# Kernel optimization log

Measured on AMD Instinct MI355X. Metric: run time of the kernel, lower is better.

Reference implementation:

```python
import jax, jax.numpy as jnp
import numpy as np

# Module hyperparameters (from init_kwargs)
C = 128        # in_channel
L = 16         # seq_len
K = 7          # filter_size
DIL = 1        # dilation
G = 4          # num_groups
SPAN = (K - 1) * DIL + 1
PAD = (SPAN - 1) // 2

B, H, W = 8, 56, 56


def setup_inputs() -> dict:
    key = jax.random.key(0)
    k1, k2 = jax.random.split(key)
    x = jax.random.normal(k1, (B, C, L, H, W), dtype=jnp.float32)
    # kaiming_normal(mode='fan_out', nonlinearity='relu'):
    # fan_out = shape[0] * K * K, std = sqrt(2 / fan_out)
    std = (2.0 / (C * K * K)) ** 0.5
    filter_weight = jax.random.normal(k2, (C, L, K, K), dtype=jnp.float32) * std
    return {"x": x, "filter_weight": filter_weight}


def reference(x, filter_weight):
    # x: (B, C, T, H, W) ; filter_weight: (C, T, K, K)
    b, c, t, h, w = x.shape
    # zero-pad spatial dims
    x2 = jnp.pad(x, ((0, 0), (0, 0), (0, 0), (PAD, PAD), (PAD, PAD)))
    # x1: temporally shifted input (frame t-1, first frame duplicated)
    x1 = jnp.concatenate([x[:, :, :1], x[:, :, :-1]], axis=2)

    outs = []
    # static K*K offset loop (dy slow, dx fast -> matches torch meshgrid 'ij' flatten order)
    for dy in range(0, SPAN, DIL):
        for dx in range(0, SPAN, DIL):
            w_ct = filter_weight[:, :, dy // DIL, dx // DIL]  # (C, T)
            shifted = jax.lax.slice(
                x2, (0, 0, 0, dy, dx), (b, c, t, dy + h, dx + w))
            prod = w_ct[None, :, :, None, None] * x1 * shifted  # (B,C,T,H,W)
            # groupwise channel mean -> (B, G, T, H, W)
            resp = prod.reshape(b, G, c // G, t, h, w).mean(axis=2)
            outs.append(resp)
    # concat over offsets along channel dim -> (B, K^2*G, T, H, W)
    return jnp.concatenate(outs, axis=1)
```

## Files before the change

kernel.cpp:

```cpp
#include <hip/hip_runtime.h>
#include <cstdint>

#define C_ 128
#define L_ 16
#define G_ 4
#define H_ 56
#define W_ 56
#define HW_ 3136
#define CH_ 4
#define NCK_ 8
#define RS_ 64
#define NROW_ 10
#define XS_F (CH_ * NROW_ * RS_)
#define XTASK_ (CH_ * NROW_ * 16)
#define WL_F 2048
#define NBUF_ 2
#define LDS_F (WL_F + NBUF_ * XS_F)

typedef float f4 __attribute__((ext_vector_type(4)));
typedef __attribute__((address_space(3))) uint32_t lds_u32;
typedef const __attribute__((address_space(1))) uint32_t glb_u32;

__global__ __launch_bounds__(256, 2)
void wcorr(const float* __restrict__ x, const float* __restrict__ wgt,
           float* __restrict__ out) {
  __shared__ float lds[LDS_F];

  int bid = blockIdx.x;
  int wid = (bid & 7) * 896 + (bid >> 3);
  int htile = wid % 14;
  int rest = wid / 14;
  int t = rest & 15;
  int bg = rest >> 4;
  int g = bg & 3;
  int b = bg >> 2;
  int h0 = htile * 4;

  int tid = threadIdx.x;
  int tx = tid & 7;
  int slot = tid >> 3;
  int h = slot & 3;
  int dy = slot >> 2;
  bool active = (dy < 7) && (tx < 7);
  int dyc = dy < 7 ? dy : 6;
  int txc = tx < 7 ? tx : 6;
  int r = h + dyc;
  int t1 = t > 0 ? t - 1 : 0;
  int w0 = 8 * txc;

  for (int i = WL_F + tid; i < LDS_F; i += 256) lds[i] = 0.0f;
  __syncthreads();

  const size_t cstride = (size_t)L_ * HW_;
  const float* xg = x + ((size_t)b * C_ + (size_t)g * 32) * cstride;
  const float* x1b = xg + (size_t)t1 * HW_ + (size_t)(h0 + h) * W_ + w0;

  {
    const float sc = 1.0f / 32.0f;
    const float* wsrc = wgt + (size_t)(g * 32) * (L_ * 49) + t * 49;
    #pragma unroll
    for (int j = 0; j < 8; ++j) {
      int idx = tid + j * 256;
      int c = idx >> 6;
      int rem = idx & 63;
      int dyy = rem >> 3, dxx = rem & 7;
      float v = 0.0f;
      if (dyy < 7 && dxx < 7)
        v = wsrc[(size_t)c * (L_ * 49) + dyy * 7 + dxx] * sc;
      lds[idx] = v;
    }
  }

  auto stage = [&](int tau, int fb, int c0, bool on) {
    int row = tau >> 4;
    int sb = tau & 15;
    int ci = (row * 205) >> 11;
    int rr = row - ci * 10;
    int vb = sb ^ (rr & 7);
    int hh = h0 - 3 + rr;
    bool ok = on && (vb >= 1) && (vb <= 14) && (hh >= 0) && (hh < H_);
    const float* src = xg + (size_t)(c0 + ci) * cstride + (size_t)t * HW_
                          + hh * W_ + (vb * 4 - 4);
    float* dst = &lds[fb + (tau & ~63) * 4];
    if (ok)
      __builtin_amdgcn_global_load_lds((glb_u32*)src, (lds_u32*)dst, 16, 0, 0);
  };
  auto stage_chunk = [&](int fb, int c0) {
    stage(tid, fb, c0, true);
    stage(tid + 256, fb, c0, true);
    stage(tid + 512, fb, c0, tid + 512 < XTASK_);
  };

  float acc[7][8];
  #pragma unroll
  for (int i = 0; i < 7; ++i)
    #pragma unroll
    for (int p = 0; p < 8; ++p) acc[i][p] = 0.0f;

  stage_chunk(WL_F, 0);

  #pragma unroll 1
  for (int k = 0; k < NCK_; ++k) {
    __syncthreads();
    if (k + 1 < NCK_)
      stage_chunk(WL_F + ((k + 1) & 1) * XS_F, (k + 1) * CH_);

    int fb = WL_F + (k & 1) * XS_F;
    int c0 = k * CH_;
    int s = r & 7;
    #pragma unroll
    for (int ci = 0; ci < CH_; ++ci) {
      const f4* xsrow = (const f4*)&lds[fb + (ci * NROW_ + r) * RS_];
      f4 q0 = xsrow[(2 * txc + 0) ^ s];
      f4 q1 = xsrow[(2 * txc + 1) ^ s];
      f4 q2 = xsrow[(2 * txc + 2) ^ s];
      f4 q3 = xsrow[(2 * txc + 3) ^ s];
      const f4* wl = (const f4*)&lds[(c0 + ci) * 64 + dyc * 8];
      f4 wv0 = wl[0];
      f4 wv1 = wl[1];
      const float* x1p = x1b + (size_t)(c0 + ci) * cstride;
      f4 a0 = *(const f4*)(x1p);
      f4 a1 = *(const f4*)(x1p + 4);
      float w7[7] = {wv0.x, wv0.y, wv0.z, wv0.w, wv1.x, wv1.y, wv1.z};
      float rr_[16] = {q0.x, q0.y, q0.z, q0.w, q1.x, q1.y, q1.z, q1.w,
                       q2.x, q2.y, q2.z, q2.w, q3.x, q3.y, q3.z, q3.w};
      float x1v[8] = {a0.x, a0.y, a0.z, a0.w, a1.x, a1.y, a1.z, a1.w};
      #pragma unroll
      for (int dxx = 0; dxx < 7; ++dxx) {
        #pragma unroll
        for (int p = 0; p < 8; ++p) {
          acc[dxx][p] = fmaf(w7[dxx], x1v[p] * rr_[p + dxx + 1], acc[dxx][p]);
        }
      }
    }
  }

  if (active) {
    #pragma unroll
    for (int dxx = 0; dxx < 7; ++dxx) {
      int och = (dy * 7 + dxx) * G_ + g;
      float* op = out + (((size_t)b * 196 + och) * L_ + t) * (size_t)HW_
                      + (size_t)(h0 + h) * W_ + w0;
      f4 o0 = {acc[dxx][0], acc[dxx][1], acc[dxx][2], acc[dxx][3]};
      f4 o1 = {acc[dxx][4], acc[dxx][5], acc[dxx][6], acc[dxx][7]};
      __builtin_nontemporal_store(o0, (f4*)op);
      __builtin_nontemporal_store(o1, (f4*)(op + 4));
    }
  }
}

extern "C" void kernel_launch(void* const* d_in, const int* in_sizes, int n_in,
                              void* d_out, int out_size, void* d_ws, size_t ws_size,
                              hipStream_t stream) {
  const float* x = (const float*)d_in[0];
  const float* w = (const float*)d_in[1];
  float* o = (float*)d_out;
  dim3 grid(7168), block(256);
  hipLaunchKernelGGL(wcorr, grid, block, 0, stream, x, w, o);
}
```

Baseline: 232.9 us.

## Give each wavefront a private LDS staging buffer and replace block barriers with vmcnt waits

Each wavefront now stages only the input rows it needs (5 rows per channel) into its own double-buffered LDS region. This removes the per-chunk __syncthreads, with each wave using s_waitcnt vmcnt to wait only on its own async global-to-LDS loads. The chunk size drops from 4 to 2 channels, and the x1 global loads are issued before staging so they overlap. Adjacent waves overlap in rows, so some input is loaded redundantly. Correctness also depends on the hand-counted vmcnt values matching the number of outstanding loads.

```diff
diff --git a/kernel.cpp b/kernel.cpp
--- a/kernel.cpp
+++ b/kernel.cpp
@@ -7,15 +7,13 @@
 #define H_ 56
 #define W_ 56
 #define HW_ 3136
-#define CH_ 4
-#define NCK_ 8
-#define RS_ 64
-#define NROW_ 10
-#define XS_F (CH_ * NROW_ * RS_)
-#define XTASK_ (CH_ * NROW_ * 16)
+#define CH_ 2
+#define NCK_ 16
+#define NR_ 5
+#define WBUF_F (CH_ * NR_ * 64)
 #define WL_F 2048
-#define NBUF_ 2
-#define LDS_F (WL_F + NBUF_ * XS_F)
+#define LDS_F (WL_F + 4 * 2 * WBUF_F)
+#define XT_ (CH_ * NR_ * 16)
 
 typedef float f4 __attribute__((ext_vector_type(4)));
 typedef __attribute__((address_space(3))) uint32_t lds_u32;
@@ -37,6 +35,8 @@
   int h0 = htile * 4;
 
   int tid = threadIdx.x;
+  int lane = tid & 63;
+  int wvu = __builtin_amdgcn_readfirstlane(tid >> 6);
   int tx = tid & 7;
   int slot = tid >> 3;
   int h = slot & 3;
@@ -45,15 +45,11 @@
   int dyc = dy < 7 ? dy : 6;
   int txc = tx < 7 ? tx : 6;
   int r = h + dyc;
+  int lr = r - 2 * wvu;
   int t1 = t > 0 ? t - 1 : 0;
   int w0 = 8 * txc;
 
   for (int i = WL_F + tid; i < LDS_F; i += 256) lds[i] = 0.0f;
-  __syncthreads();
-
-  const size_t cstride = (size_t)L_ * HW_;
-  const float* xg = x + ((size_t)b * C_ + (size_t)g * 32) * cstride;
-  const float* x1b = xg + (size_t)t1 * HW_ + (size_t)(h0 + h) * W_ + w0;
 
   {
     const float sc = 1.0f / 32.0f;
@@ -71,24 +67,26 @@
     }
   }
 
-  auto stage = [&](int tau, int fb, int c0, bool on) {
+  const size_t cstride = (size_t)L_ * HW_;
+  const float* xg = x + ((size_t)b * C_ + (size_t)g * 32) * cstride;
+  const float* x1b = xg + (size_t)t1 * HW_ + (size_t)(h0 + h) * W_ + w0;
+
+  auto stage = [&](int call, int kb, int c0) {
+    int tau = lane + call * 64;
     int row = tau >> 4;
     int sb = tau & 15;
-    int ci = (row * 205) >> 11;
-    int rr = row - ci * 10;
-    int vb = sb ^ (rr & 7);
-    int hh = h0 - 3 + rr;
-    bool ok = on && (vb >= 1) && (vb <= 14) && (hh >= 0) && (hh < H_);
+    int ci = (row >= NR_) ? 1 : 0;
+    int lrr = row - ci * NR_;
+    int rg = 2 * wvu + lrr;
+    int vb = sb ^ (rg & 7);
+    int hh = h0 - 3 + rg;
+    bool ok = (tau < XT_) && (vb >= 1) && (vb <= 14) && (rg <= 9)
+              && (hh >= 0) && (hh < H_);
     const float* src = xg + (size_t)(c0 + ci) * cstride + (size_t)t * HW_
                           + hh * W_ + (vb * 4 - 4);
-    float* dst = &lds[fb + (tau & ~63) * 4];
+    float* dst = &lds[WL_F + (wvu * 2 + kb) * WBUF_F + call * 256];
     if (ok)
       __builtin_amdgcn_global_load_lds((glb_u32*)src, (lds_u32*)dst, 16, 0, 0);
-  };
-  auto stage_chunk = [&](int fb, int c0) {
-    stage(tid, fb, c0, true);
-    stage(tid + 256, fb, c0, true);
-    stage(tid + 512, fb, c0, tid + 512 < XTASK_);
   };
 
   float acc[7][8];
@@ -97,20 +95,36 @@
     #pragma unroll
     for (int p = 0; p < 8; ++p) acc[i][p] = 0.0f;
 
-  stage_chunk(WL_F, 0);
+  __syncthreads();
 
+  stage(0, 0, 0); stage(1, 0, 0); stage(2, 0, 0);
+
+  int s = r & 7;
   #pragma unroll 1
   for (int k = 0; k < NCK_; ++k) {
-    __syncthreads();
-    if (k + 1 < NCK_)
-      stage_chunk(WL_F + ((k + 1) & 1) * XS_F, (k + 1) * CH_);
+    __builtin_amdgcn_sched_barrier(0);
+    int c0 = k * CH_;
+    int kb = k & 1;
+    const float* x1p0 = x1b + (size_t)(c0 + 0) * cstride;
+    const float* x1p1 = x1b + (size_t)(c0 + 1) * cstride;
+    f4 a00 = *(const f4*)(x1p0);
+    f4 a01 = *(const f4*)(x1p0 + 4);
+    f4 a10 = *(const f4*)(x1p1);
+    f4 a11 = *(const f4*)(x1p1 + 4);
+    if (k + 1 < NCK_) {
+      stage(0, kb ^ 1, c0 + CH_);
+      stage(1, kb ^ 1, c0 + CH_);
+      stage(2, kb ^ 1, c0 + CH_);
+      asm volatile("s_waitcnt vmcnt(6)");
+    } else {
+      asm volatile("s_waitcnt vmcnt(4)");
+    }
+    __builtin_amdgcn_sched_barrier(0);
 
-    int fb = WL_F + (k & 1) * XS_F;
-    int c0 = k * CH_;
-    int s = r & 7;
+    const float* base = &lds[WL_F + (wvu * 2 + kb) * WBUF_F];
     #pragma unroll
     for (int ci = 0; ci < CH_; ++ci) {
-      const f4* xsrow = (const f4*)&lds[fb + (ci * NROW_ + r) * RS_];
+      const f4* xsrow = (const f4*)(base + (ci * NR_ + lr) * 64);
       f4 q0 = xsrow[(2 * txc + 0) ^ s];
       f4 q1 = xsrow[(2 * txc + 1) ^ s];
       f4 q2 = xsrow[(2 * txc + 2) ^ s];
@@ -118,9 +132,8 @@
       const f4* wl = (const f4*)&lds[(c0 + ci) * 64 + dyc * 8];
       f4 wv0 = wl[0];
       f4 wv1 = wl[1];
-      const float* x1p = x1b + (size_t)(c0 + ci) * cstride;
-      f4 a0 = *(const f4*)(x1p);
-      f4 a1 = *(const f4*)(x1p + 4);
+      f4 a0 = ci ? a10 : a00;
+      f4 a1 = ci ? a11 : a01;
       float w7[7] = {wv0.x, wv0.y, wv0.z, wv0.w, wv1.x, wv1.y, wv1.z};
       float rr_[16] = {q0.x, q0.y, q0.z, q0.w, q1.x, q1.y, q1.z, q1.w,
                        q2.x, q2.y, q2.z, q2.w, q3.x, q3.y, q3.z, q3.w};
```

New measurement: 220.4 us. 1.06x faster.

## Replace LDS-staged shifted input with direct per-thread global loads and zero-pad pointer

Applied to the files above, without the earlier changes.

Drops the double-buffered LDS staging of padded input rows through global_load_lds and its per-chunk barriers. Each thread now loads its shifted row segments straight from global memory. Out-of-bounds padding loads are redirected to a zeroed workspace buffer with a zero stride, which avoids branches. This cuts LDS traffic and synchronisation, but relies on L1/L2 to catch the heavy reuse across dy rows, so redundant global loads go up. It also adds a memset launch.

```diff
diff --git a/kernel.cpp b/kernel.cpp
--- a/kernel.cpp
+++ b/kernel.cpp
@@ -7,24 +7,14 @@
 #define H_ 56
 #define W_ 56
 #define HW_ 3136
-#define CH_ 4
-#define NCK_ 8
-#define RS_ 64
-#define NROW_ 10
-#define XS_F (CH_ * NROW_ * RS_)
-#define XTASK_ (CH_ * NROW_ * 16)
 #define WL_F 2048
-#define NBUF_ 2
-#define LDS_F (WL_F + NBUF_ * XS_F)
 
 typedef float f4 __attribute__((ext_vector_type(4)));
-typedef __attribute__((address_space(3))) uint32_t lds_u32;
-typedef const __attribute__((address_space(1))) uint32_t glb_u32;
 
 __global__ __launch_bounds__(256, 2)
 void wcorr(const float* __restrict__ x, const float* __restrict__ wgt,
-           float* __restrict__ out) {
-  __shared__ float lds[LDS_F];
+           float* __restrict__ out, const float* __restrict__ zsrc) {
+  __shared__ float lds[WL_F];
 
   int bid = blockIdx.x;
   int wid = (bid & 7) * 896 + (bid >> 3);
@@ -44,16 +34,31 @@
   bool active = (dy < 7) && (tx < 7);
   int dyc = dy < 7 ? dy : 6;
   int txc = tx < 7 ? tx : 6;
-  int r = h + dyc;
   int t1 = t > 0 ? t - 1 : 0;
   int w0 = 8 * txc;
-
-  for (int i = WL_F + tid; i < LDS_F; i += 256) lds[i] = 0.0f;
-  __syncthreads();
+  int hh = h0 + h + dyc - 3;
+  bool hv = (hh >= 0) && (hh < H_);
 
   const size_t cstride = (size_t)L_ * HW_;
   const float* xg = x + ((size_t)b * C_ + (size_t)g * 32) * cstride;
-  const float* x1b = xg + (size_t)t1 * HW_ + (size_t)(h0 + h) * W_ + w0;
+
+  const float* xsbase = xg + (size_t)t * HW_ + (size_t)(hv ? hh : 0) * W_;
+  const float *p0, *p1, *p2, *p3;
+  ptrdiff_t i0, i1, i2, i3;
+  {
+    bool v0 = hv && (w0 >= 4);
+    bool v3 = hv && (w0 + 8 < W_);
+    p0 = v0 ? xsbase + (w0 - 4) : zsrc + (tid & 15) * 4;
+    p1 = hv ? xsbase + w0       : zsrc + (tid & 15) * 4;
+    p2 = hv ? xsbase + (w0 + 4) : zsrc + (tid & 15) * 4;
+    p3 = v3 ? xsbase + (w0 + 8) : zsrc + (tid & 15) * 4;
+    i0 = v0 ? (ptrdiff_t)cstride : 0;
+    i1 = hv ? (ptrdiff_t)cstride : 0;
+    i2 = hv ? (ptrdiff_t)cstride : 0;
+    i3 = v3 ? (ptrdiff_t)cstride : 0;
+  }
+  const float* pa = xg + (size_t)t1 * HW_ + (size_t)(h0 + h) * W_ + w0;
+  const float* pb = pa + 4;
 
   {
     const float sc = 1.0f / 32.0f;
@@ -71,66 +76,38 @@
     }
   }
 
-  auto stage = [&](int tau, int fb, int c0, bool on) {
-    int row = tau >> 4;
-    int sb = tau & 15;
-    int ci = (row * 205) >> 11;
-    int rr = row - ci * 10;
-    int vb = sb ^ (rr & 7);
-    int hh = h0 - 3 + rr;
-    bool ok = on && (vb >= 1) && (vb <= 14) && (hh >= 0) && (hh < H_);
-    const float* src = xg + (size_t)(c0 + ci) * cstride + (size_t)t * HW_
-                          + hh * W_ + (vb * 4 - 4);
-    float* dst = &lds[fb + (tau & ~63) * 4];
-    if (ok)
-      __builtin_amdgcn_global_load_lds((glb_u32*)src, (lds_u32*)dst, 16, 0, 0);
-  };
-  auto stage_chunk = [&](int fb, int c0) {
-    stage(tid, fb, c0, true);
-    stage(tid + 256, fb, c0, true);
-    stage(tid + 512, fb, c0, tid + 512 < XTASK_);
-  };
-
   float acc[7][8];
   #pragma unroll
   for (int i = 0; i < 7; ++i)
     #pragma unroll
     for (int p = 0; p < 8; ++p) acc[i][p] = 0.0f;
 
-  stage_chunk(WL_F, 0);
+  __syncthreads();
 
-  #pragma unroll 1
-  for (int k = 0; k < NCK_; ++k) {
-    __syncthreads();
-    if (k + 1 < NCK_)
-      stage_chunk(WL_F + ((k + 1) & 1) * XS_F, (k + 1) * CH_);
+  #pragma unroll 2
+  for (int c = 0; c < 32; ++c) {
+    f4 q0 = *(const f4*)p0;
+    f4 q1 = *(const f4*)p1;
+    f4 q2 = *(const f4*)p2;
+    f4 q3 = *(const f4*)p3;
+    f4 a0 = *(const f4*)pa;
+    f4 a1 = *(const f4*)pb;
+    p0 += i0; p1 += i1; p2 += i2; p3 += i3;
+    pa += cstride; pb += cstride;
 
-    int fb = WL_F + (k & 1) * XS_F;
-    int c0 = k * CH_;
-    int s = r & 7;
+    const f4* wl = (const f4*)&lds[c * 64 + dyc * 8];
+    f4 W0 = wl[0], W1 = wl[1];
+    float w7[7] = {W0.x, W0.y, W0.z, W0.w, W1.x, W1.y, W1.z};
+
+    float rr_[16] = {q0.x, q0.y, q0.z, q0.w, q1.x, q1.y, q1.z, q1.w,
+                     q2.x, q2.y, q2.z, q2.w, q3.x, q3.y, q3.z, q3.w};
+    float x1v[8] = {a0.x, a0.y, a0.z, a0.w, a1.x, a1.y, a1.z, a1.w};
+
     #pragma unroll
-    for (int ci = 0; ci < CH_; ++ci) {
-      const f4* xsrow = (const f4*)&lds[fb + (ci * NROW_ + r) * RS_];
-      f4 q0 = xsrow[(2 * txc + 0) ^ s];
-      f4 q1 = xsrow[(2 * txc + 1) ^ s];
-      f4 q2 = xsrow[(2 * txc + 2) ^ s];
-      f4 q3 = xsrow[(2 * txc + 3) ^ s];
-      const f4* wl = (const f4*)&lds[(c0 + ci) * 64 + dyc * 8];
-      f4 wv0 = wl[0];
-      f4 wv1 = wl[1];
-      const float* x1p = x1b + (size_t)(c0 + ci) * cstride;
-      f4 a0 = *(const f4*)(x1p);
-      f4 a1 = *(const f4*)(x1p + 4);
-      float w7[7] = {wv0.x, wv0.y, wv0.z, wv0.w, wv1.x, wv1.y, wv1.z};
-      float rr_[16] = {q0.x, q0.y, q0.z, q0.w, q1.x, q1.y, q1.z, q1.w,
-                       q2.x, q2.y, q2.z, q2.w, q3.x, q3.y, q3.z, q3.w};
-      float x1v[8] = {a0.x, a0.y, a0.z, a0.w, a1.x, a1.y, a1.z, a1.w};
+    for (int dxx = 0; dxx < 7; ++dxx) {
       #pragma unroll
-      for (int dxx = 0; dxx < 7; ++dxx) {
-        #pragma unroll
-        for (int p = 0; p < 8; ++p) {
-          acc[dxx][p] = fmaf(w7[dxx], x1v[p] * rr_[p + dxx + 1], acc[dxx][p]);
-        }
+      for (int p = 0; p < 8; ++p) {
+        acc[dxx][p] = fmaf(w7[dxx], x1v[p] * rr_[p + dxx + 1], acc[dxx][p]);
       }
     }
   }
@@ -155,6 +132,7 @@
   const float* x = (const float*)d_in[0];
   const float* w = (const float*)d_in[1];
   float* o = (float*)d_out;
+  hipMemsetAsync(d_ws, 0, 256, stream);
   dim3 grid(7168), block(256);
-  hipLaunchKernelGGL(wcorr, grid, block, 0, stream, x, w, o);
+  hipLaunchKernelGGL(wcorr, grid, block, 0, stream, x, w, o, (const float*)d_ws);
 }
```

Measured after the change: 318.0 us. 36.5% more time.
